# Kernel tuning notes

Hardware: AMD Instinct MI355X
Metric: run time of the kernel (lower is better)

Reference implementation:

```python
import jax, jax.numpy as jnp
import numpy as np

TOP_K = 8
N_EXPERTS = 64
ALPHA = 0.001
EPS = 1e-9


def setup_inputs() -> dict:
    key = jax.random.key(0)
    k1, k2 = jax.random.split(key)
    B, S, H, E = 4, 4096, 2048, N_EXPERTS
    hidden_states = jax.random.normal(k1, (B, S, H), dtype=jnp.float32)
    # kaiming_uniform_(a=sqrt(5)) on [E,H] -> bound = 1/sqrt(H)
    bound = 1.0 / np.sqrt(H)
    weight = jax.random.uniform(k2, (E, H), dtype=jnp.float32, minval=-bound, maxval=bound)
    return {"hidden_states": hidden_states, "weight": weight}


def reference(hidden_states, weight):
    B, S, H = hidden_states.shape
    E = weight.shape[0]
    x = hidden_states.reshape(-1, H)                     # [N, H], N = B*S
    logits = jnp.einsum('nh,eh->ne', x, weight)          # [N, E]
    scores = jax.nn.sigmoid(logits)                      # sigmoid affinity (DeepSeek-V3 style)

    topk_weight, topk_idx = jax.lax.top_k(scores, TOP_K)  # [N, K]
    # norm_topk_prob = True and top_k > 1
    denom = topk_weight.sum(axis=-1, keepdims=True) + EPS
    topk_weight = topk_weight / denom

    # aux load-balance loss (training, alpha > 0); scatter-count instead of one_hot
    N = x.shape[0]
    counts = jnp.zeros((E,), dtype=jnp.float32).at[topk_idx.reshape(-1)].add(1.0)
    load = counts / (N * TOP_K)                          # == one_hot.mean(dim=(0,1))
    prob_raw = scores / (scores.sum(axis=-1, keepdims=True) + EPS)
    prob = prob_raw.mean(axis=0)
    prob = prob / (prob.sum() + EPS)
    aux_loss = ALPHA * (load * prob).sum() * E

    return topk_idx, topk_weight, aux_loss
```

## Files before the change

### kernel.cpp

```cpp
#include <hip/hip_runtime.h>
#include <math.h>

#define N_TOK 16384
#define HDIM  2048
#define NEXP  64
#define TOPK  8
#define NKS   4
#define KSEG  (HDIM / NKS)
#define KCH   32
#define NCH   (KSEG / KCH)

#define PART_OFF  0
#define STATS_OFF (33u << 20)

typedef double d4 __attribute__((ext_vector_type(4)));

__global__ void mfma_probe_kernel(int* __restrict__ flag) {
    const int l = threadIdx.x;
    const int i16 = l & 15, q = l >> 4;
    const int r4 = l >> 2,  m4 = l & 3;
    int fv = 0;
#pragma unroll
    for (int ai = 0; ai < 2; ++ai)
#pragma unroll
    for (int bi = 0; bi < 2; ++bi) {
        const int ra = ai ? r4 : i16, ka = ai ? m4 : q;
        const int cb = bi ? r4 : i16, kb = bi ? m4 : q;
        double a = (double)(ra * 4 + ka + 1);
        double b = (double)((kb + 1) * 100 + 3 * cb);
        d4 acc = {0., 0., 0., 0.};
        acc = __builtin_amdgcn_mfma_f64_16x16x4f64(a, b, acc, 0, 0, 0);
#pragma unroll
        for (int sf = 0; sf < 2; ++sf)
#pragma unroll
        for (int tr = 0; tr < 2; ++tr) {
            int ok = 1;
#pragma unroll
            for (int r = 0; r < 4; ++r) {
                const int p   = sf ? (q + 4 * r) : (4 * q + r);
                const int row = tr ? i16 : p;
                const int col = tr ? p : i16;
                double ref = 0.0;
#pragma unroll
                for (int k = 0; k < 4; ++k)
                    ref += (double)(row * 4 + k + 1) * (double)((k + 1) * 100 + 3 * col);
                ok &= (acc[r] == ref);
            }
            if (__all(ok) && fv == 0) fv = 1 + ai * 8 + bi * 4 + sf * 2 + tr;
        }
    }
    if (l == 0) *flag = fv;
}

__global__ __launch_bounds__(512, 8) void gemm_mfma_kernel(const float* __restrict__ X,
                                                           const float* __restrict__ W,
                                                           const int* __restrict__ flag,
                                                           double* __restrict__ part) {
    const int f = *flag;
    if (f == 0) return;
    const int fb = f - 1;
    const int ai = (fb >> 3) & 1, bi = (fb >> 2) & 1;
    const int sf = (fb >> 1) & 1, tr = fb & 1;

    const int tt  = blockIdx.x >> 2;
    const int ks  = blockIdx.x & 3;
    const int tid = threadIdx.x;
    const int l   = tid & 63;
    const int wv  = tid >> 6;
    const int wr  = wv >> 2;
    const int wc  = wv & 3;
    const int tok0 = tt * 64;
    const int k0   = ks * KSEG;

    const int i16 = l & 15, q = l >> 4, r4 = l >> 2, m4 = l & 3;
    const int ra = ai ? r4 : i16, ka = ai ? m4 : q;
    const int cb = bi ? r4 : i16, kb = bi ? m4 : q;

    __shared__ double Xs[64][34];
    __shared__ double Ws[64][34];

    d4 acc0 = {0., 0., 0., 0.};
    d4 acc1 = {0., 0., 0., 0.};

    const int sr = tid >> 3;
    const int sc = (tid & 7) * 4;
    const float* xg = X + (size_t)(tok0 + sr) * HDIM + k0 + sc;
    const float* wg = W + (size_t)sr * HDIM + k0 + sc;

    float4 px = *(const float4*)xg;
    float4 pw = *(const float4*)wg;

    for (int c = 0; c < NCH; ++c) {
        __syncthreads();
        {
            double2 d0, d1;
            d0.x = (double)px.x; d0.y = (double)px.y;
            d1.x = (double)px.z; d1.y = (double)px.w;
            *(double2*)&Xs[sr][sc]     = d0;
            *(double2*)&Xs[sr][sc + 2] = d1;
            d0.x = (double)pw.x; d0.y = (double)pw.y;
            d1.x = (double)pw.z; d1.y = (double)pw.w;
            *(double2*)&Ws[sr][sc]     = d0;
            *(double2*)&Ws[sr][sc + 2] = d1;
        }
        __syncthreads();
        if (c + 1 < NCH) {
            px = *(const float4*)(xg + (c + 1) * KCH);
            pw = *(const float4*)(wg + (c + 1) * KCH);
        }
        const double* pa0 = &Xs[wr * 32 + ra][ka];
        const double* pa1 = &Xs[wr * 32 + 16 + ra][ka];
        const double* pb0 = &Ws[wc * 16 + cb][kb];
#pragma unroll
        for (int kq = 0; kq < 8; ++kq) {
            double a0 = pa0[4 * kq];
            double a1 = pa1[4 * kq];
            double b0 = pb0[4 * kq];
            acc0 = __builtin_amdgcn_mfma_f64_16x16x4f64(a0, b0, acc0, 0, 0, 0);
            acc1 = __builtin_amdgcn_mfma_f64_16x16x4f64(a1, b0, acc1, 0, 0, 0);
        }
    }

    double* pbase = part + (size_t)ks * N_TOK * NEXP;
#pragma unroll
    for (int rt = 0; rt < 2; ++rt) {
        const d4 accv = rt == 0 ? acc0 : acc1;
#pragma unroll
        for (int r = 0; r < 4; ++r) {
            const int p    = sf ? (q + 4 * r) : (4 * q + r);
            const int dtok = tr ? i16 : p;
            const int dex  = tr ? p : i16;
            const int tok  = tok0 + wr * 32 + rt * 16 + dtok;
            const int ex   = wc * 16 + dex;
            pbase[(size_t)tok * NEXP + ex] = accv[r];
        }
    }
}

__global__ __launch_bounds__(512, 4) void gemm_valu_kernel(const float* __restrict__ X,
                                                           const float* __restrict__ W,
                                                           const int* __restrict__ flag,
                                                           double* __restrict__ part) {
    if (*flag != 0) return;
    const int tt   = blockIdx.x >> 2;
    const int ks   = blockIdx.x & 3;
    const int tid  = threadIdx.x;
    const int lane = tid & 63;
    const int wv   = tid >> 6;
    const int tok0 = tt * 64;
    const int k0   = ks * KSEG;

    __shared__ double xs[64][18];
    __shared__ double wsh[16][66];

    double acc[8];
#pragma unroll
    for (int t = 0; t < 8; ++t) acc[t] = 0.0;

    const int sx_tok = tid >> 3;
    const int sx_k   = (tid & 7) * 2;
    const float* xg  = X + (size_t)(tok0 + sx_tok) * HDIM + k0 + sx_k;
    const int sw_k = tid >> 5;
    const int sw_e = (tid & 31) * 2;
    const float* wg0 = W + (size_t)sw_e * HDIM + k0 + sw_k;
    const float* wg1 = W + (size_t)(sw_e + 1) * HDIM + k0 + sw_k;

    float2 px = *(const float2*)xg;
    float  pa = *wg0, pb2 = *wg1;

    for (int c = 0; c < KSEG / 16; ++c) {
        __syncthreads();
        {
            double2 xv; xv.x = (double)px.x; xv.y = (double)px.y;
            *(double2*)&xs[sx_tok][sx_k] = xv;
            double2 wv2; wv2.x = (double)pa; wv2.y = (double)pb2;
            *(double2*)&wsh[sw_k][sw_e] = wv2;
        }
        __syncthreads();
        if (c + 1 < KSEG / 16) {
            px  = *(const float2*)(xg + (c + 1) * 16);
            pa  = wg0[(c + 1) * 16];
            pb2 = wg1[(c + 1) * 16];
        }
        double wr_[16];
#pragma unroll
        for (int j = 0; j < 16; ++j) wr_[j] = wsh[j][lane];
#pragma unroll
        for (int t = 0; t < 8; ++t) {
            const int trr = wv * 8 + t;
#pragma unroll
            for (int kp = 0; kp < 8; ++kp) {
                double2 xv = *(const double2*)&xs[trr][kp * 2];
                acc[t] = fma(xv.x, wr_[kp * 2],     acc[t]);
                acc[t] = fma(xv.y, wr_[kp * 2 + 1], acc[t]);
            }
        }
    }

    double* pb = part + ((size_t)ks * N_TOK + tok0 + wv * 8) * NEXP + lane;
#pragma unroll
    for (int t = 0; t < 8; ++t)
        pb[(size_t)t * NEXP] = acc[t];
}

__global__ __launch_bounds__(256) void topk_kernel(const double* __restrict__ part,
                                                   float* __restrict__ outIdx,
                                                   float* __restrict__ outW,
                                                   float* __restrict__ stats) {
    __shared__ float sc_s[32][65];
    __shared__ float lds_counts[NEXP];
    __shared__ float psum_part[4][NEXP];
    const int tid  = threadIdx.x;
    const int lane = tid & 63;
    const int w    = tid >> 6;
    if (tid < NEXP) lds_counts[tid] = 0.f;

    const int t0 = blockIdx.x * 32;
#pragma unroll
    for (int p = 0; p < 8; ++p) {
        const int idx = p * 256 + tid;
        const int t   = idx >> 6;
        const int e   = idx & 63;
        const double* pp = part + ((size_t)(t0 + t)) * NEXP + e;
        double l = (pp[0] + pp[(size_t)N_TOK * NEXP]) +
                   (pp[2 * (size_t)N_TOK * NEXP] + pp[3 * (size_t)N_TOK * NEXP]);
        sc_s[t][e] = (float)(1.0 / (1.0 + exp(-l)));
    }
    __syncthreads();

    float ps = 0.f;
    for (int i = 0; i < 8; ++i) {
        const int tloc = w * 8 + i;
        const int t    = t0 + tloc;
        float s = sc_s[tloc][lane];

        float rs = s;
#pragma unroll
        for (int off = 32; off; off >>= 1) rs += __shfl_xor(rs, off);
        ps += s / (rs + 1e-9f);

        float cur = s;
        float denom = 0.f;
        int   wi = 0;
        float wvv = 0.f;
#pragma unroll
        for (int k = 0; k < TOPK; ++k) {
            float m = cur; int mi = lane;
#pragma unroll
            for (int off = 32; off; off >>= 1) {
                float om = __shfl_xor(m, off);
                int   oi = __shfl_xor(mi, off);
                if (om > m || (om == m && oi < mi)) { m = om; mi = oi; }
            }
            denom += m;
            if (lane == k)  { wi = mi; wvv = m; }
            if (lane == mi) cur = -1e30f;
        }
        if (lane < TOPK) {
            outIdx[(size_t)t * TOPK + lane] = (float)wi;
            outW  [(size_t)t * TOPK + lane] = wvv / (denom + 1e-9f);
            atomicAdd(&lds_counts[wi], 1.f);
        }
    }
    psum_part[w][lane] = ps;
    __syncthreads();
    if (tid < NEXP) {
        float tot = psum_part[0][tid] + psum_part[1][tid] +
                    psum_part[2][tid] + psum_part[3][tid];
        atomicAdd(&stats[tid], tot);
        atomicAdd(&stats[NEXP + tid], lds_counts[tid]);
    }
}

__global__ void aux_kernel(const float* __restrict__ stats, float* __restrict__ out) {
    const int e = threadIdx.x;
    float prob = stats[e] / (float)N_TOK;
    float cnt  = stats[NEXP + e];
    float loadf = cnt / ((float)N_TOK * TOPK);
    float S = prob;
#pragma unroll
    for (int off = 32; off; off >>= 1) S += __shfl_xor(S, off);
    float pn = prob / (S + 1e-9f);
    float v  = loadf * pn;
#pragma unroll
    for (int off = 32; off; off >>= 1) v += __shfl_xor(v, off);
    if (e == 0) out[2 * N_TOK * TOPK] = 0.001f * v * (float)NEXP;
}

extern "C" void kernel_launch(void* const* d_in, const int* in_sizes, int n_in,
                              void* d_out, int out_size, void* d_ws, size_t ws_size,
                              hipStream_t stream) {
    (void)in_sizes; (void)n_in; (void)out_size; (void)ws_size;
    const float* X = (const float*)d_in[0];
    const float* W = (const float*)d_in[1];
    float* out = (float*)d_out;
    char*  ws  = (char*)d_ws;
    double* part  = (double*)(ws + PART_OFF);
    float*  stats = (float*)(ws + STATS_OFF);
    int*    flag  = (int*)(stats + 128);

    hipMemsetAsync(stats, 0, 132 * sizeof(float), stream);
    mfma_probe_kernel<<<1, 64, 0, stream>>>(flag);
    gemm_mfma_kernel<<<1024, 512, 0, stream>>>(X, W, flag, part);
    gemm_valu_kernel<<<1024, 512, 0, stream>>>(X, W, flag, part);
    topk_kernel<<<512, 256, 0, stream>>>(part, out, out + N_TOK * TOPK, stats);
    aux_kernel<<<1, 64, 0, stream>>>(stats, out);
}
```

Measured before the change: 140.7 us.

## Inline MFMA layout probe, swizzle LDS tiles, fold aux loss into topk

Removes the separate probe kernel by having every wave derive the MFMA layout flag inline. It also removes the aux kernel by having the last topk block, found through an atomic counter, compute the aux loss. The LDS tiles lose their padding and use an XOR swizzle on columns to avoid bank conflicts. Together these cut two kernel launches and the padded LDS footprint. In exchange, every block now runs a few extra MFMA probe instructions and the topk kernel gains a threadfence and a last-block check.

```diff
diff --git a/kernel.cpp b/kernel.cpp
--- a/kernel.cpp
+++ b/kernel.cpp
@@ -15,8 +15,10 @@
 
 typedef double d4 __attribute__((ext_vector_type(4)));
 
-__global__ void mfma_probe_kernel(int* __restrict__ flag) {
-    const int l = threadIdx.x;
+#define SWZ(r) ((((r) & 3) << 2) | ((((r) >> 2) & 1) << 1))
+
+__device__ __forceinline__ int derive_flag() {
+    const int l = threadIdx.x & 63;
     const int i16 = l & 15, q = l >> 4;
     const int r4 = l >> 2,  m4 = l & 3;
     int fv = 0;
@@ -49,14 +51,13 @@
             if (__all(ok) && fv == 0) fv = 1 + ai * 8 + bi * 4 + sf * 2 + tr;
         }
     }
-    if (l == 0) *flag = fv;
+    return fv;
 }
 
 __global__ __launch_bounds__(512, 8) void gemm_mfma_kernel(const float* __restrict__ X,
                                                            const float* __restrict__ W,
-                                                           const int* __restrict__ flag,
                                                            double* __restrict__ part) {
-    const int f = *flag;
+    const int f = derive_flag();
     if (f == 0) return;
     const int fb = f - 1;
     const int ai = (fb >> 3) & 1, bi = (fb >> 2) & 1;
@@ -76,19 +77,30 @@
     const int ra = ai ? r4 : i16, ka = ai ? m4 : q;
     const int cb = bi ? r4 : i16, kb = bi ? m4 : q;
 
-    __shared__ double Xs[64][34];
-    __shared__ double Ws[64][34];
+    __shared__ double Xs[64][32];
+    __shared__ double Ws[64][32];
 
     d4 acc0 = {0., 0., 0., 0.};
     d4 acc1 = {0., 0., 0., 0.};
 
-    const int sr = tid >> 3;
-    const int sc = (tid & 7) * 4;
-    const float* xg = X + (size_t)(tok0 + sr) * HDIM + k0 + sc;
-    const float* wg = W + (size_t)sr * HDIM + k0 + sc;
+    const int sr  = tid >> 3;
+    const int s_w = SWZ(sr);
+    const int cb0 = (4 * (tid & 7)) ^ (s_w & 12);
+    const int cA  = cb0 + (0 ^ (s_w & 2));
+    const int cB  = cb0 + (2 ^ (s_w & 2));
+    const float* xg = X + (size_t)(tok0 + sr) * HDIM + k0 + 4 * (tid & 7);
+    const float* wg = W + (size_t)sr * HDIM + k0 + 4 * (tid & 7);
 
     float4 px = *(const float4*)xg;
     float4 pw = *(const float4*)wg;
+
+    const int sa = SWZ(ra & 7);
+    const int sb = SWZ(cb & 7);
+    const int caL = ka ^ (sa & 2);
+    const int cbL = kb ^ (sb & 2);
+    const double* rowA0 = &Xs[wr * 32 + ra][0];
+    const double* rowA1 = &Xs[wr * 32 + 16 + ra][0];
+    const double* rowB  = &Ws[wc * 16 + cb][0];
 
     for (int c = 0; c < NCH; ++c) {
         __syncthreads();
@@ -96,26 +108,25 @@
             double2 d0, d1;
             d0.x = (double)px.x; d0.y = (double)px.y;
             d1.x = (double)px.z; d1.y = (double)px.w;
-            *(double2*)&Xs[sr][sc]     = d0;
-            *(double2*)&Xs[sr][sc + 2] = d1;
+            *(double2*)&Xs[sr][cA] = d0;
+            *(double2*)&Xs[sr][cB] = d1;
             d0.x = (double)pw.x; d0.y = (double)pw.y;
             d1.x = (double)pw.z; d1.y = (double)pw.w;
-            *(double2*)&Ws[sr][sc]     = d0;
-            *(double2*)&Ws[sr][sc + 2] = d1;
+            *(double2*)&Ws[sr][cA] = d0;
+            *(double2*)&Ws[sr][cB] = d1;
         }
         __syncthreads();
         if (c + 1 < NCH) {
             px = *(const float4*)(xg + (c + 1) * KCH);
             pw = *(const float4*)(wg + (c + 1) * KCH);
         }
-        const double* pa0 = &Xs[wr * 32 + ra][ka];
-        const double* pa1 = &Xs[wr * 32 + 16 + ra][ka];
-        const double* pb0 = &Ws[wc * 16 + cb][kb];
 #pragma unroll
         for (int kq = 0; kq < 8; ++kq) {
-            double a0 = pa0[4 * kq];
-            double a1 = pa1[4 * kq];
-            double b0 = pb0[4 * kq];
+            const int ca  = ((4 * kq) ^ (sa & 12)) + caL;
+            const int cbb = ((4 * kq) ^ (sb & 12)) + cbL;
+            double a0 = rowA0[ca];
+            double a1 = rowA1[ca];
+            double b0 = rowB[cbb];
             acc0 = __builtin_amdgcn_mfma_f64_16x16x4f64(a0, b0, acc0, 0, 0, 0);
             acc1 = __builtin_amdgcn_mfma_f64_16x16x4f64(a1, b0, acc1, 0, 0, 0);
         }
@@ -139,9 +150,8 @@
 
 __global__ __launch_bounds__(512, 4) void gemm_valu_kernel(const float* __restrict__ X,
                                                            const float* __restrict__ W,
-                                                           const int* __restrict__ flag,
                                                            double* __restrict__ part) {
-    if (*flag != 0) return;
+    if (derive_flag() != 0) return;
     const int tt   = blockIdx.x >> 2;
     const int ks   = blockIdx.x & 3;
     const int tid  = threadIdx.x;
@@ -206,10 +216,13 @@
 __global__ __launch_bounds__(256) void topk_kernel(const double* __restrict__ part,
                                                    float* __restrict__ outIdx,
                                                    float* __restrict__ outW,
-                                                   float* __restrict__ stats) {
+                                                   float* __restrict__ stats,
+                                                   unsigned* __restrict__ cnt,
+                                                   float* __restrict__ auxOut) {
     __shared__ float sc_s[32][65];
     __shared__ float lds_counts[NEXP];
     __shared__ float psum_part[4][NEXP];
+    __shared__ int   isLast;
     const int tid  = threadIdx.x;
     const int lane = tid & 63;
     const int w    = tid >> 6;
@@ -270,21 +283,26 @@
         atomicAdd(&stats[tid], tot);
         atomicAdd(&stats[NEXP + tid], lds_counts[tid]);
     }
-}
-
-__global__ void aux_kernel(const float* __restrict__ stats, float* __restrict__ out) {
-    const int e = threadIdx.x;
-    float prob = stats[e] / (float)N_TOK;
-    float cnt  = stats[NEXP + e];
-    float loadf = cnt / ((float)N_TOK * TOPK);
-    float S = prob;
-#pragma unroll
-    for (int off = 32; off; off >>= 1) S += __shfl_xor(S, off);
-    float pn = prob / (S + 1e-9f);
-    float v  = loadf * pn;
-#pragma unroll
-    for (int off = 32; off; off >>= 1) v += __shfl_xor(v, off);
-    if (e == 0) out[2 * N_TOK * TOPK] = 0.001f * v * (float)NEXP;
+    __threadfence();
+    __syncthreads();
+    if (tid == 0) {
+        unsigned old = atomicAdd(cnt, 1u);
+        isLast = (old == (unsigned)(gridDim.x - 1));
+    }
+    __syncthreads();
+    if (isLast && tid < 64) {
+        float prob = atomicAdd(&stats[tid], 0.f) / (float)N_TOK;
+        float c    = atomicAdd(&stats[NEXP + tid], 0.f);
+        float loadf = c / ((float)N_TOK * TOPK);
+        float S = prob;
+#pragma unroll
+        for (int off = 32; off; off >>= 1) S += __shfl_xor(S, off);
+        float pn = prob / (S + 1e-9f);
+        float v  = loadf * pn;
+#pragma unroll
+        for (int off = 32; off; off >>= 1) v += __shfl_xor(v, off);
+        if (tid == 0) auxOut[0] = 0.001f * v * (float)NEXP;
+    }
 }
 
 extern "C" void kernel_launch(void* const* d_in, const int* in_sizes, int n_in,
@@ -295,14 +313,13 @@
     const float* W = (const float*)d_in[1];
     float* out = (float*)d_out;
     char*  ws  = (char*)d_ws;
-    double* part  = (double*)(ws + PART_OFF);
-    float*  stats = (float*)(ws + STATS_OFF);
-    int*    flag  = (int*)(stats + 128);
+    double*   part  = (double*)(ws + PART_OFF);
+    float*    stats = (float*)(ws + STATS_OFF);
+    unsigned* cnt   = (unsigned*)(stats + 128);
 
     hipMemsetAsync(stats, 0, 132 * sizeof(float), stream);
-    mfma_probe_kernel<<<1, 64, 0, stream>>>(flag);
-    gemm_mfma_kernel<<<1024, 512, 0, stream>>>(X, W, flag, part);
-    gemm_valu_kernel<<<1024, 512, 0, stream>>>(X, W, flag, part);
-    topk_kernel<<<512, 256, 0, stream>>>(part, out, out + N_TOK * TOPK, stats);
-    aux_kernel<<<1, 64, 0, stream>>>(stats, out);
-}
+    gemm_mfma_kernel<<<1024, 512, 0, stream>>>(X, W, part);
+    gemm_valu_kernel<<<1024, 512, 0, stream>>>(X, W, part);
+    topk_kernel<<<512, 256, 0, stream>>>(part, out, out + N_TOK * TOPK, stats,
+                                         cnt, out + 2 * N_TOK * TOPK);
+}
```

After: 180.4 us. 28.2% more time.
